# Optimization experiments

Hardware: AMD Instinct MI355X
Metric: run time of the kernel (lower is better)

The kernel has to match this reference:

```python
import jax, jax.numpy as jnp
import numpy as np

B, N, D_MODEL, D_INNER = 8, 1024, 512, 2048
N_HEAD, D_K, D_V = 8, 64, 64
N_EXPERTS, TOP_K = 24, 2
N_GROUPS = 4
EPS = 1e-6


def setup_inputs() -> dict:
    key = jax.random.key(0)
    ks = jax.random.split(key, 12)
    s = 0.02
    rn = lambda k, shp: jax.random.normal(k, shp, dtype=jnp.float32) * s
    inp = {
        "x": jax.random.normal(ks[0], (B, N, D_MODEL), dtype=jnp.float32),
        "wq": rn(ks[1], (D_MODEL, N_HEAD * D_K)),
        "wk": rn(ks[2], (D_MODEL, N_HEAD * D_K)),
        "wv": rn(ks[3], (D_MODEL, N_HEAD * D_V)),
        "wo": rn(ks[4], (N_HEAD * D_V, D_MODEL)),
        "ln_attn_g": jnp.ones((D_MODEL,), jnp.float32),
        "ln_attn_b": jnp.zeros((D_MODEL,), jnp.float32),
        "wg1": rn(ks[5], (D_MODEL, N_EXPERTS)),
        "w1": rn(ks[6], (N_EXPERTS, D_MODEL, D_INNER)),
        "b1": jnp.zeros((N_EXPERTS, D_INNER), jnp.float32),
        "wg2": rn(ks[7], (D_INNER, N_EXPERTS)),
        "w2": rn(ks[8], (N_EXPERTS, D_INNER, D_MODEL)),
        "b2": jnp.zeros((N_EXPERTS, D_MODEL), jnp.float32),
        "ln_out_g": jnp.ones((D_MODEL,), jnp.float32),
        "ln_out_b": jnp.zeros((D_MODEL,), jnp.float32),
    }
    for i in range(1, 5):
        inp[f"ln{i}_g"] = jnp.ones((D_INNER,), jnp.float32)
        inp[f"ln{i}_b"] = jnp.zeros((D_INNER,), jnp.float32)
    return inp


def _ln(x, g, b):
    m = jnp.mean(x, -1, keepdims=True)
    v = jnp.mean((x - m) ** 2, -1, keepdims=True)
    return (x - m) * jax.lax.rsqrt(v + EPS) * g + b


def _gate(xf, wg, capacity):
    # top-2 gating with capacity-limited one-hot dispatch (GShard-style)
    gates = jax.nn.softmax(xf @ wg)                      # [T,E]
    w, idx = jax.lax.top_k(gates, TOP_K)                 # [T,2]
    w = w / jnp.sum(w, -1, keepdims=True)
    m1 = jax.nn.one_hot(idx[:, 0], N_EXPERTS, dtype=xf.dtype)
    m2 = jax.nn.one_hot(idx[:, 1], N_EXPERTS, dtype=xf.dtype)
    loc1 = jnp.cumsum(m1, 0) - 1.0                       # slot within expert
    loc2 = jnp.cumsum(m2, 0) - 1.0 + jnp.sum(m1, 0)[None, :]
    m1 = m1 * (loc1 < capacity)
    m2 = m2 * (loc2 < capacity)
    c1 = w[:, 0, None, None] * m1[:, :, None] * jax.nn.one_hot(loc1.astype(jnp.int32), capacity, dtype=xf.dtype)
    c2 = w[:, 1, None, None] * m2[:, :, None] * jax.nn.one_hot(loc2.astype(jnp.int32), capacity, dtype=xf.dtype)
    combine = c1 + c2                                    # [T,E,C]
    dispatch = (combine > 0).astype(xf.dtype)
    return combine, dispatch


def _moe(xf, combine, dispatch, W, b):
    ein = jnp.einsum('tec,td->ecd', dispatch, xf)        # gather into expert slots
    out = jnp.einsum('ecd,edh->ech', ein, W) + b[:, None, :]
    return jnp.einsum('tec,ech->th', combine, out)       # weighted combine


def reference(x, wq, wk, wv, wo, ln_attn_g, ln_attn_b, wg1, w1, b1, wg2, w2, b2,
              ln1_g, ln1_b, ln2_g, ln2_b, ln3_g, ln3_b, ln4_g, ln4_b,
              ln_out_g, ln_out_b):
    # ---- multi-head self-attention ----
    temp = D_K ** 0.5
    q = (x @ wq).reshape(B, N, N_HEAD, D_K)
    k = (x @ wk).reshape(B, N, N_HEAD, D_K)
    v = (x @ wv).reshape(B, N, N_HEAD, D_V)
    attn = jax.nn.softmax(jnp.einsum('bnhd,bmhd->bhnm', q / temp, k), axis=-1)
    ctx = jnp.einsum('bhnm,bmhd->bnhd', attn, v).reshape(B, N, N_HEAD * D_V)
    ctx = jax.nn.relu(ctx @ wo) + x                      # dropout is identity at eval
    ctx = _ln(ctx, ln_attn_g, ln_attn_b)
    # ---- TaskMoE positionwise FFN over 4 sequence groups ----
    resid = ctx
    xg = ctx.reshape(B, N_GROUPS, N // N_GROUPS, D_MODEL)
    T = B * (N // N_GROUPS)
    cap = int(np.ceil(T * TOP_K / N_EXPERTS))
    ln_gs = [ln1_g, ln2_g, ln3_g, ln4_g]
    ln_bs = [ln1_b, ln2_b, ln3_b, ln4_b]
    outs = []
    for i in range(N_GROUPS):
        xf = xg[:, i].reshape(T, D_MODEL)
        combine, dispatch = _gate(xf, wg1, cap)          # routing reused by 2nd MoE
        h = _moe(xf, combine, dispatch, w1, b1)          # [T, D_INNER]
        h = jax.nn.relu(_ln(h, ln_gs[i], ln_bs[i]))
        o = _moe(h, combine, dispatch, w2, b2)           # [T, D_MODEL]
        outs.append(o.reshape(B, N // N_GROUPS, D_MODEL))
    y = jnp.concatenate(outs, axis=1) + resid
    return _ln(y, ln_out_g, ln_out_b)
```

## Files before the change

kernel.cpp:

```cpp
#include <hip/hip_runtime.h>
#include <cstdint>


#define NTOK 8192
#define DM   512
#define DI   2048
#define NEXP 24
#define TPG  2048
#define CAP  171
#define CAPR 176
#define EPSF 1e-6f

typedef __bf16 bf16x8 __attribute__((ext_vector_type(8)));
typedef float f32x4 __attribute__((ext_vector_type(4)));

static __device__ __forceinline__ unsigned short f2bf(float f) {
  unsigned int u = __builtin_bit_cast(unsigned int, f);
  u = (u + 0x7fffu + ((u >> 16) & 1u)) >> 16;
  return (unsigned short)u;
}
static __device__ __forceinline__ unsigned int pk2(float a, float b) {
  return (unsigned int)f2bf(a) | ((unsigned int)f2bf(b) << 16);
}

static __device__ __forceinline__ void gload16(const unsigned short* g, unsigned short* l) {
  __builtin_amdgcn_global_load_lds(
      (const __attribute__((address_space(1))) void*)g,
      (__attribute__((address_space(3))) void*)l, 16, 0, 0);
}

__global__ __launch_bounds__(256) void convw(
    const float* __restrict__ in, unsigned short* __restrict__ out, int K, int N)
{
  __shared__ unsigned short T[64][65];
  int e = blockIdx.z;
  const float* ip = in + (size_t)e * K * N;
  unsigned short* op = out + (size_t)e * N * K;
  int n0 = blockIdx.x * 64, k0 = blockIdx.y * 64;
  int tid = threadIdx.x;
  #pragma unroll
  for (int i = 0; i < 16; ++i) {
    int lin = tid + i * 256;
    int k = lin >> 6, n = lin & 63;
    T[n][k] = f2bf(ip[(size_t)(k0 + k) * N + n0 + n]);
  }
  __syncthreads();
  #pragma unroll
  for (int i = 0; i < 16; ++i) {
    int lin = tid + i * 256;
    int n = lin >> 6, k = lin & 63;
    op[(size_t)(n0 + n) * K + k0 + k] = T[n][k];
  }
}

__global__ __launch_bounds__(256) void convx(
    const float* __restrict__ in, unsigned short* __restrict__ out)
{
  int i = blockIdx.x * 256 + threadIdx.x;
  float4 v = ((const float4*)in)[i];
  uint2 p;
  p.x = pk2(v.x, v.y); p.y = pk2(v.z, v.w);
  ((uint2*)out)[i] = p;
}

__global__ __launch_bounds__(256) void mfma_gemm(
    const unsigned short* __restrict__ A, int lda,
    const unsigned short* __restrict__ Bt,
    const float* __restrict__ bias,
    const int* __restrict__ lrow, const float* __restrict__ lw,
    const int* __restrict__ cnts,
    float* __restrict__ Cf, unsigned short* __restrict__ Cb,
    const float* __restrict__ Add,
    int M, int N, int K, int mode, float scale)
{
  __shared__ unsigned short As[2][64 * 64];
  __shared__ unsigned short Bs[2][128 * 64];
  int tid = threadIdx.x;
  int w = tid >> 6, lane = tid & 63, quad = lane >> 4, l16 = lane & 15;
  int n0 = blockIdx.x * 128;
  int m0 = blockIdx.y * 64;
  int pair = blockIdx.z;
  int e = pair % NEXP;
  int count = cnts ? cnts[pair] : M;
  if (m0 >= count) return;
  const int*   lr  = lrow ? lrow + pair * CAPR : nullptr;
  const float* lwp = lw   ? lw   + pair * CAPR : nullptr;

  int sub = lane >> 3;
  int gsw = (lane & 7) ^ sub;
  const unsigned short* aSrc[2];
  #pragma unroll
  for (int i = 0; i < 2; ++i) {
    int mm = m0 + i * 32 + w * 8 + sub;
    if (mm >= count) mm = count - 1;
    int rm = lr ? lr[mm] : mm;
    aSrc[i] = A + (size_t)rm * lda + gsw * 8;
  }
  const unsigned short* Bte = Bt + (size_t)e * N * K;
  const unsigned short* bSrc[4];
  #pragma unroll
  for (int i = 0; i < 4; ++i)
    bSrc[i] = Bte + (size_t)(n0 + i * 32 + w * 8 + sub) * K + gsw * 8;

  int wbase = w * 512;

  f32x4 acc[4][2] = {};
  int nt = K >> 6;

  #pragma unroll
  for (int i = 0; i < 2; ++i) gload16(aSrc[i], &As[0][i * 2048 + wbase]);
  #pragma unroll
  for (int i = 0; i < 4; ++i) gload16(bSrc[i], &Bs[0][i * 2048 + wbase]);

  for (int t = 0; t < nt; ++t) {
    asm volatile("s_waitcnt vmcnt(0)" ::: "memory");
    __syncthreads();
    int cur = t & 1;
    if (t + 1 < nt) {
      int koff = (t + 1) << 6;
      int nxt = cur ^ 1;
      #pragma unroll
      for (int i = 0; i < 2; ++i) gload16(aSrc[i] + koff, &As[nxt][i * 2048 + wbase]);
      #pragma unroll
      for (int i = 0; i < 4; ++i) gload16(bSrc[i] + koff, &Bs[nxt][i * 2048 + wbase]);
    }
    const unsigned short* Ab = As[cur];
    const unsigned short* Bb = Bs[cur];
    #pragma unroll
    for (int half = 0; half < 2; ++half) {
      int g8 = ((half * 4 + quad) ^ (l16 & 7)) * 8;
      bf16x8 af[4];
      #pragma unroll
      for (int ms = 0; ms < 4; ++ms)
        af[ms] = *(const bf16x8*)&Ab[(ms * 16 + l16) * 64 + g8];
      bf16x8 bfr[2];
      #pragma unroll
      for (int ns = 0; ns < 2; ++ns)
        bfr[ns] = *(const bf16x8*)&Bb[(w * 32 + ns * 16 + l16) * 64 + g8];
      #pragma unroll
      for (int ms = 0; ms < 4; ++ms)
        #pragma unroll
        for (int ns = 0; ns < 2; ++ns)
          acc[ms][ns] = __builtin_amdgcn_mfma_f32_16x16x32_bf16(af[ms], bfr[ns], acc[ms][ns], 0, 0, 0);
    }
  }
  float bv[2];
  if (mode == 2) {
    #pragma unroll
    for (int ns = 0; ns < 2; ++ns)
      bv[ns] = bias[(size_t)e * N + n0 + w * 32 + ns * 16 + l16];
  }
  #pragma unroll
  for (int ms = 0; ms < 4; ++ms) {
    #pragma unroll
    for (int ns = 0; ns < 2; ++ns) {
      int col = n0 + w * 32 + ns * 16 + l16;
      #pragma unroll
      for (int r = 0; r < 4; ++r) {
        int m = m0 + ms * 16 + quad * 4 + r;
        if (mode == 0) {
          Cb[(size_t)m * N + col] = f2bf(acc[ms][ns][r] * scale);
        } else if (mode == 1) {
          Cf[(size_t)m * N + col] = fmaxf(acc[ms][ns][r], 0.f) + Add[(size_t)m * N + col];
        } else {
          if (m < count) {
            int rr = lr[m];
            float wgt = lwp[m];
            atomicAdd(&Cf[(size_t)rr * N + col], wgt * (acc[ms][ns][r] + bv[ns]));
          }
        }
      }
    }
  }
}

__global__ __launch_bounds__(256) void attn_mfma(
    const unsigned short* __restrict__ Qb, const unsigned short* __restrict__ Kb,
    const unsigned short* __restrict__ Vb, unsigned short* __restrict__ ctx)
{
  __shared__ unsigned short Ks[64 * 72];
  __shared__ unsigned short Vt[64 * 72];
  __shared__ unsigned short Ps[4][16 * 72];
  int tid = threadIdx.x;
  int w = tid >> 6, lane = tid & 63, quad = lane >> 4, l16 = lane & 15;
  int qt = blockIdx.x, bh = blockIdx.y;
  int b = bh >> 3, h = bh & 7;
  size_t hoff = (size_t)h * 64;
  size_t tokbase = (size_t)b * 1024;

  int qrow = qt * 64 + w * 16 + l16;
  const unsigned short* qp = Qb + (tokbase + qrow) * 512 + hoff + quad * 8;
  bf16x8 qa0 = *(const bf16x8*)(qp);
  bf16x8 qa1 = *(const bf16x8*)(qp + 32);

  f32x4 O[4] = {};
  float mrow[4], lrowv[4];
  #pragma unroll
  for (int r = 0; r < 4; ++r) { mrow[r] = -1e30f; lrowv[r] = 0.f; }

  for (int kv0 = 0; kv0 < 1024; kv0 += 64) {
    __syncthreads();
    {
      const unsigned short* kg = Kb + (tokbase + kv0) * 512 + hoff;
      #pragma unroll
      for (int i = 0; i < 2; ++i) {
        int f = tid + i * 256;
        int key = f >> 3, c = f & 7;
        *(uint4*)&Ks[key * 72 + c * 8] = *(const uint4*)(kg + (size_t)key * 512 + c * 8);
      }
      const unsigned short* vg = Vb + (tokbase + kv0) * 512 + hoff;
      int d = tid & 63;
      #pragma unroll
      for (int i = 0; i < 2; ++i) {
        int ko = (tid >> 6) + i * 4;
        const unsigned short* vq = vg + (size_t)ko * 8 * 512 + d;
        unsigned int a0 = vq[0],        a1 = vq[512];
        unsigned int a2 = vq[2 * 512],  a3 = vq[3 * 512];
        unsigned int a4 = vq[4 * 512],  a5 = vq[5 * 512];
        unsigned int a6 = vq[6 * 512],  a7 = vq[7 * 512];
        uint4 pk;
        pk.x = a0 | (a1 << 16); pk.y = a2 | (a3 << 16);
        pk.z = a4 | (a5 << 16); pk.w = a6 | (a7 << 16);
        *(uint4*)&Vt[d * 72 + ko * 8] = pk;
      }
    }
    __syncthreads();

    f32x4 s[4];
    #pragma unroll
    for (int kt = 0; kt < 4; ++kt) {
      const unsigned short* kr = &Ks[(kt * 16 + l16) * 72 + quad * 8];
      bf16x8 kb0 = *(const bf16x8*)(kr);
      bf16x8 kb1 = *(const bf16x8*)(kr + 32);
      f32x4 z = {};
      z = __builtin_amdgcn_mfma_f32_16x16x32_bf16(qa0, kb0, z, 0, 0, 0);
      z = __builtin_amdgcn_mfma_f32_16x16x32_bf16(qa1, kb1, z, 0, 0, 0);
      s[kt] = z;
    }

    #pragma unroll
    for (int r = 0; r < 4; ++r) {
      float mx = fmaxf(fmaxf(s[0][r], s[1][r]), fmaxf(s[2][r], s[3][r]));
      mx = fmaxf(mx, __shfl_xor(mx, 1, 64));
      mx = fmaxf(mx, __shfl_xor(mx, 2, 64));
      mx = fmaxf(mx, __shfl_xor(mx, 4, 64));
      mx = fmaxf(mx, __shfl_xor(mx, 8, 64));
      float mnew = fmaxf(mrow[r], mx);
      float alpha = __expf(mrow[r] - mnew);
      mrow[r] = mnew;
      float psum = 0.f;
      #pragma unroll
      for (int kt = 0; kt < 4; ++kt) {
        float p = __expf(s[kt][r] - mnew);
        s[kt][r] = p;
        psum += p;
      }
      psum += __shfl_xor(psum, 1, 64);
      psum += __shfl_xor(psum, 2, 64);
      psum += __shfl_xor(psum, 4, 64);
      psum += __shfl_xor(psum, 8, 64);
      lrowv[r] = lrowv[r] * alpha + psum;
      #pragma unroll
      for (int dt = 0; dt < 4; ++dt) O[dt][r] *= alpha;
    }

    #pragma unroll
    for (int kt = 0; kt < 4; ++kt)
      #pragma unroll
      for (int r = 0; r < 4; ++r)
        Ps[w][(quad * 4 + r) * 72 + kt * 16 + l16] = f2bf(s[kt][r]);
    const unsigned short* pp = &Ps[w][l16 * 72 + quad * 8];
    bf16x8 pa0 = *(const bf16x8*)(pp);
    bf16x8 pa1 = *(const bf16x8*)(pp + 32);

    #pragma unroll
    for (int dt = 0; dt < 4; ++dt) {
      const unsigned short* vr = &Vt[(dt * 16 + l16) * 72 + quad * 8];
      bf16x8 vb0 = *(const bf16x8*)(vr);
      bf16x8 vb1 = *(const bf16x8*)(vr + 32);
      O[dt] = __builtin_amdgcn_mfma_f32_16x16x32_bf16(pa0, vb0, O[dt], 0, 0, 0);
      O[dt] = __builtin_amdgcn_mfma_f32_16x16x32_bf16(pa1, vb1, O[dt], 0, 0, 0);
    }
  }

  #pragma unroll
  for (int r = 0; r < 4; ++r) {
    float inv = 1.0f / lrowv[r];
    int row = qt * 64 + w * 16 + quad * 4 + r;
    unsigned short* cp = ctx + (tokbase + row) * 512 + hoff + l16;
    #pragma unroll
    for (int dt = 0; dt < 4; ++dt) cp[dt * 16] = f2bf(O[dt][r] * inv);
  }
}

__global__ __launch_bounds__(256) void ln_kernel(
    const float* __restrict__ in, const float* __restrict__ add,
    float* __restrict__ out, unsigned short* __restrict__ outb,
    int D, int relu_after,
    const float* __restrict__ g0, const float* __restrict__ g1,
    const float* __restrict__ g2, const float* __restrict__ g3,
    const float* __restrict__ bb0, const float* __restrict__ bb1,
    const float* __restrict__ bb2, const float* __restrict__ bb3)
{
  int row = blockIdx.x;
  int grp = (row & 1023) >> 8;
  const float* g  = grp == 0 ? g0  : grp == 1 ? g1  : grp == 2 ? g2  : g3;
  const float* bb = grp == 0 ? bb0 : grp == 1 ? bb1 : grp == 2 ? bb2 : bb3;
  const float* ip = in + (size_t)row * D;
  const float* ap = add ? add + (size_t)row * D : nullptr;
  float vals[8];
  int per = D >> 8;
  float s1 = 0.f, s2 = 0.f;
  for (int i = 0; i < per; ++i) {
    int d = threadIdx.x + (i << 8);
    float vv = ip[d];
    if (ap) vv += ap[d];
    vals[i] = vv; s1 += vv; s2 += vv * vv;
  }
  #pragma unroll
  for (int o = 32; o; o >>= 1) { s1 += __shfl_xor(s1, o, 64); s2 += __shfl_xor(s2, o, 64); }
  __shared__ float sA[4], sB[4];
  int wid = threadIdx.x >> 6, lane = threadIdx.x & 63;
  if (lane == 0) { sA[wid] = s1; sB[wid] = s2; }
  __syncthreads();
  float t1 = sA[0] + sA[1] + sA[2] + sA[3];
  float t2 = sB[0] + sB[1] + sB[2] + sB[3];
  float mean = t1 / (float)D;
  float var = t2 / (float)D - mean * mean;
  float rs = rsqrtf(var + EPSF);
  float* op = out ? out + (size_t)row * D : nullptr;
  unsigned short* obp = outb ? outb + (size_t)row * D : nullptr;
  for (int i = 0; i < per; ++i) {
    int d = threadIdx.x + (i << 8);
    float o = (vals[i] - mean) * rs * g[d] + bb[d];
    if (relu_after) o = fmaxf(o, 0.f);
    if (op)  op[d] = o;
    if (obp) obp[d] = f2bf(o);
  }
}

__global__ __launch_bounds__(256) void gate1(
    const float* __restrict__ xln, const float* __restrict__ wg,
    int* __restrict__ idx0, int* __restrict__ idx1,
    float* __restrict__ w0o, float* __restrict__ w1o)
{
  int wid = threadIdx.x >> 6, lane = threadIdx.x & 63;
  int tk = blockIdx.x * 4 + wid;
  int g = tk >> 11, t = tk & 2047;
  int b = t >> 8, j = t & 255;
  size_t row = (size_t)b * 1024 + g * 256 + j;
  const float* xp = xln + row * 512;
  float acc = -1e30f;
  if (lane < 24) {
    acc = 0.f;
    for (int d = 0; d < 512; ++d) acc += xp[d] * wg[d * 24 + lane];
  }
  float b0v = -1e30f, b1v = -1e30f; int i0 = 0, i1 = 0;
  for (int e = 0; e < 24; ++e) {
    float vv = __shfl(acc, e, 64);
    if (vv > b0v)      { b1v = b0v; i1 = i0; b0v = vv; i0 = e; }
    else if (vv > b1v) { b1v = vv; i1 = e; }
  }
  if (lane == 0) {
    float w0 = 1.0f / (1.0f + __expf(b1v - b0v));
    idx0[tk] = i0; idx1[tk] = i1; w0o[tk] = w0; w1o[tk] = 1.0f - w0;
  }
}

__global__ __launch_bounds__(64) void gate2(
    const int* __restrict__ idx0, const int* __restrict__ idx1,
    const float* __restrict__ w0, const float* __restrict__ w1,
    int* __restrict__ lrow, float* __restrict__ lw, int* __restrict__ counts)
{
  int pair = blockIdx.x; int g = pair / 24; int e = pair % 24;
  int lane = threadIdx.x;
  int base = g * TPG;
  unsigned long long lm = (lane == 63) ? 0x7fffffffffffffffULL : ((1ULL << lane) - 1ULL);
  int run = 0;
  for (int it = 0; it < TPG / 64; ++it) {
    int t = it * 64 + lane;
    bool m = (idx0[base + t] == e);
    unsigned long long mask = __ballot(m);
    int pre = __popcll(mask & lm);
    int rank = run + pre;
    if (m && rank < CAP) {
      int bq = t >> 8, j = t & 255;
      lrow[pair * CAPR + rank] = bq * 1024 + g * 256 + j;
      lw[pair * CAPR + rank] = w0[base + t];
    }
    run += __popcll(mask);
  }
  int total1 = run;
  int run2 = 0;
  for (int it = 0; it < TPG / 64; ++it) {
    int t = it * 64 + lane;
    bool m = (idx1[base + t] == e);
    unsigned long long mask = __ballot(m);
    int pre = __popcll(mask & lm);
    int rank2 = run2 + pre;
    if (m && (total1 + rank2) < CAP) {
      int bq = t >> 8, j = t & 255;
      lrow[pair * CAPR + total1 + rank2] = bq * 1024 + g * 256 + j;
      lw[pair * CAPR + total1 + rank2] = w1[base + t];
    }
    run2 += __popcll(mask);
  }
  if (lane == 0) {
    int c1 = total1 < CAP ? total1 : CAP;
    int room = CAP - total1; if (room < 0) room = 0;
    int c2 = run2 < room ? run2 : room;
    counts[pair] = c1 + c2;
  }
}

extern "C" void kernel_launch(void* const* d_in, const int* in_sizes, int n_in,
                              void* d_out, int out_size, void* d_ws, size_t ws_size,
                              hipStream_t stream)
{
  const float* x   = (const float*)d_in[0];
  const float* wq  = (const float*)d_in[1];
  const float* wk  = (const float*)d_in[2];
  const float* wv  = (const float*)d_in[3];
  const float* wo  = (const float*)d_in[4];
  const float* ln_attn_g = (const float*)d_in[5];
  const float* ln_attn_b = (const float*)d_in[6];
  const float* wg1 = (const float*)d_in[7];
  const float* w1  = (const float*)d_in[8];
  const float* b1  = (const float*)d_in[9];
  const float* w2  = (const float*)d_in[11];
  const float* b2  = (const float*)d_in[12];
  const float* ln_out_g = (const float*)d_in[13];
  const float* ln_out_b = (const float*)d_in[14];
  const float* ln1g = (const float*)d_in[15]; const float* ln1b = (const float*)d_in[16];
  const float* ln2g = (const float*)d_in[17]; const float* ln2b = (const float*)d_in[18];
  const float* ln3g = (const float*)d_in[19]; const float* ln3b = (const float*)d_in[20];
  const float* ln4g = (const float*)d_in[21]; const float* ln4b = (const float*)d_in[22];

  char* ws = (char*)d_ws;
  const size_t MB = 1048576;
  unsigned short* wt1  = (unsigned short*)(ws + 0);
  unsigned short* wtq  = (unsigned short*)(ws + 48 * MB);
  unsigned short* wtk  = (unsigned short*)(ws + 48 * MB + 524288);
  unsigned short* wtv  = (unsigned short*)(ws + 49 * MB);
  unsigned short* wto  = (unsigned short*)(ws + 49 * MB + 524288);
  unsigned short* xbf  = (unsigned short*)(ws + 50 * MB);
  unsigned short* hb2  = (unsigned short*)(ws + 50 * MB);
  unsigned short* qbf  = (unsigned short*)(ws + 58 * MB);
  unsigned short* kbf  = (unsigned short*)(ws + 66 * MB);
  unsigned short* vbf  = (unsigned short*)(ws + 74 * MB);
  unsigned short* ctxb = (unsigned short*)(ws + 82 * MB);
  float* y0    = (float*)(ws + 90 * MB);
  float* ymoe  = (float*)(ws + 90 * MB);
  float* ctxln = (float*)(ws + 106 * MB);
  unsigned short* ctxlnb = (unsigned short*)(ws + 122 * MB);
  float* hb    = (float*)(ws + 130 * MB);
  unsigned short* wt2 = (unsigned short*)(ws + 130 * MB);
  char*  small = ws + 194 * MB;
  int*   idx0  = (int*)(small + 0);
  int*   idx1  = (int*)(small + 32768);
  float* w0a   = (float*)(small + 65536);
  float* w1a   = (float*)(small + 98304);
  int*   lrowp = (int*)(small + 131072);
  float* lwv   = (float*)(small + 198656);
  int*   cnts  = (int*)(small + 266240);

  dim3 blk(256);
  convw<<<dim3(8, 8, 1), blk, 0, stream>>>(wq, wtq, 512, 512);
  convw<<<dim3(8, 8, 1), blk, 0, stream>>>(wk, wtk, 512, 512);
  convw<<<dim3(8, 8, 1), blk, 0, stream>>>(wv, wtv, 512, 512);
  convw<<<dim3(8, 8, 1), blk, 0, stream>>>(wo, wto, 512, 512);
  convw<<<dim3(32, 8, 24), blk, 0, stream>>>(w1, wt1, 512, 2048);
  convx<<<4096, blk, 0, stream>>>(x, xbf);
  mfma_gemm<<<dim3(4, 128, 1), blk, 0, stream>>>(xbf, DM, wtq, nullptr, nullptr, nullptr, nullptr,
      nullptr, qbf, nullptr, NTOK, DM, DM, 0, 0.125f);
  mfma_gemm<<<dim3(4, 128, 1), blk, 0, stream>>>(xbf, DM, wtk, nullptr, nullptr, nullptr, nullptr,
      nullptr, kbf, nullptr, NTOK, DM, DM, 0, 1.0f);
  mfma_gemm<<<dim3(4, 128, 1), blk, 0, stream>>>(xbf, DM, wtv, nullptr, nullptr, nullptr, nullptr,
      nullptr, vbf, nullptr, NTOK, DM, DM, 0, 1.0f);
  attn_mfma<<<dim3(16, 64), blk, 0, stream>>>(qbf, kbf, vbf, ctxb);
  mfma_gemm<<<dim3(4, 128, 1), blk, 0, stream>>>(ctxb, DM, wto, nullptr, nullptr, nullptr, nullptr,
      y0, nullptr, x, NTOK, DM, DM, 1, 1.0f);
  ln_kernel<<<8192, blk, 0, stream>>>(y0, nullptr, ctxln, ctxlnb, DM, 0,
      ln_attn_g, ln_attn_g, ln_attn_g, ln_attn_g, ln_attn_b, ln_attn_b, ln_attn_b, ln_attn_b);
  gate1<<<2048, blk, 0, stream>>>(ctxln, wg1, idx0, idx1, w0a, w1a);
  gate2<<<96, 64, 0, stream>>>(idx0, idx1, w0a, w1a, lrowp, lwv, cnts);
  hipMemsetAsync(hb, 0, (size_t)NTOK * DI * 4, stream);
  hipMemsetAsync(ymoe, 0, (size_t)NTOK * DM * 4, stream);
  mfma_gemm<<<dim3(16, 3, 96), blk, 0, stream>>>(ctxlnb, DM, wt1, b1, lrowp, lwv, cnts,
      hb, nullptr, nullptr, 0, DI, DM, 2, 1.0f);
  ln_kernel<<<8192, blk, 0, stream>>>(hb, nullptr, nullptr, hb2, DI, 1,
      ln1g, ln2g, ln3g, ln4g, ln1b, ln2b, ln3b, ln4b);
  convw<<<dim3(8, 32, 24), blk, 0, stream>>>(w2, wt2, 2048, 512);
  mfma_gemm<<<dim3(4, 3, 96), blk, 0, stream>>>(hb2, DI, wt2, b2, lrowp, lwv, cnts,
      ymoe, nullptr, nullptr, 0, DM, DI, 2, 1.0f);
  ln_kernel<<<8192, blk, 0, stream>>>(ymoe, ctxln, (float*)d_out, nullptr, DM, 0,
      ln_out_g, ln_out_g, ln_out_g, ln_out_g, ln_out_b, ln_out_b, ln_out_b, ln_out_b);
}
```

Baseline: 829.8 us.

## Replace atomic MoE scatter with slot buffers and gather-combine fused into layernorm

The expert GEMMs now write bf16 per-slot outputs instead of atomically adding weighted results into zeroed fp32 token buffers. New combine_ln kernels gather each token's two slots through token-to-slot maps built in gate2, apply the gate weights and residual, and run the layernorm in the same pass. This removes the large memsets and the atomic traffic. The Q/K/V projections are also merged into one GEMM with a packed 1536-wide output that attention reads directly. The GEMM drops its double-buffered LDS prefetch for a simpler load-wait-compute loop, which may expose memory latency, and the intermediate expert outputs are rounded to bf16 before combining.

```diff
diff --git a/kernel.cpp b/kernel.cpp
--- a/kernel.cpp
+++ b/kernel.cpp
@@ -19,6 +19,9 @@
   u = (u + 0x7fffu + ((u >> 16) & 1u)) >> 16;
   return (unsigned short)u;
 }
+static __device__ __forceinline__ float bf2f(unsigned short u) {
+  return __builtin_bit_cast(float, (unsigned int)u << 16);
+}
 static __device__ __forceinline__ unsigned int pk2(float a, float b) {
   return (unsigned int)f2bf(a) | ((unsigned int)f2bf(b) << 16);
 }
@@ -67,14 +70,13 @@
     const unsigned short* __restrict__ A, int lda,
     const unsigned short* __restrict__ Bt,
     const float* __restrict__ bias,
-    const int* __restrict__ lrow, const float* __restrict__ lw,
-    const int* __restrict__ cnts,
+    const int* __restrict__ lrow, const int* __restrict__ cnts,
     float* __restrict__ Cf, unsigned short* __restrict__ Cb,
     const float* __restrict__ Add,
     int M, int N, int K, int mode, float scale)
 {
-  __shared__ unsigned short As[2][64 * 64];
-  __shared__ unsigned short Bs[2][128 * 64];
+  __shared__ unsigned short As[64 * 64];
+  __shared__ unsigned short Bs[128 * 64];
   int tid = threadIdx.x;
   int w = tid >> 6, lane = tid & 63, quad = lane >> 4, l16 = lane & 15;
   int n0 = blockIdx.x * 128;
@@ -83,8 +85,7 @@
   int e = pair % NEXP;
   int count = cnts ? cnts[pair] : M;
   if (m0 >= count) return;
-  const int*   lr  = lrow ? lrow + pair * CAPR : nullptr;
-  const float* lwp = lw   ? lw   + pair * CAPR : nullptr;
+  const int* lr = lrow ? lrow + pair * CAPR : nullptr;
 
   int sub = lane >> 3;
   int gsw = (lane & 7) ^ sub;
@@ -105,38 +106,25 @@
   int wbase = w * 512;
 
   f32x4 acc[4][2] = {};
-  int nt = K >> 6;
-
-  #pragma unroll
-  for (int i = 0; i < 2; ++i) gload16(aSrc[i], &As[0][i * 2048 + wbase]);
-  #pragma unroll
-  for (int i = 0; i < 4; ++i) gload16(bSrc[i], &Bs[0][i * 2048 + wbase]);
-
-  for (int t = 0; t < nt; ++t) {
+  for (int t = 0; t < K; t += 64) {
+    if (t) __syncthreads();
+    #pragma unroll
+    for (int i = 0; i < 2; ++i) gload16(aSrc[i] + t, &As[i * 2048 + wbase]);
+    #pragma unroll
+    for (int i = 0; i < 4; ++i) gload16(bSrc[i] + t, &Bs[i * 2048 + wbase]);
     asm volatile("s_waitcnt vmcnt(0)" ::: "memory");
     __syncthreads();
-    int cur = t & 1;
-    if (t + 1 < nt) {
-      int koff = (t + 1) << 6;
-      int nxt = cur ^ 1;
-      #pragma unroll
-      for (int i = 0; i < 2; ++i) gload16(aSrc[i] + koff, &As[nxt][i * 2048 + wbase]);
-      #pragma unroll
-      for (int i = 0; i < 4; ++i) gload16(bSrc[i] + koff, &Bs[nxt][i * 2048 + wbase]);
-    }
-    const unsigned short* Ab = As[cur];
-    const unsigned short* Bb = Bs[cur];
     #pragma unroll
     for (int half = 0; half < 2; ++half) {
       int g8 = ((half * 4 + quad) ^ (l16 & 7)) * 8;
       bf16x8 af[4];
       #pragma unroll
       for (int ms = 0; ms < 4; ++ms)
-        af[ms] = *(const bf16x8*)&Ab[(ms * 16 + l16) * 64 + g8];
+        af[ms] = *(const bf16x8*)&As[(ms * 16 + l16) * 64 + g8];
       bf16x8 bfr[2];
       #pragma unroll
       for (int ns = 0; ns < 2; ++ns)
-        bfr[ns] = *(const bf16x8*)&Bb[(w * 32 + ns * 16 + l16) * 64 + g8];
+        bfr[ns] = *(const bf16x8*)&Bs[(w * 32 + ns * 16 + l16) * 64 + g8];
       #pragma unroll
       for (int ms = 0; ms < 4; ++ms)
         #pragma unroll
@@ -144,11 +132,13 @@
           acc[ms][ns] = __builtin_amdgcn_mfma_f32_16x16x32_bf16(af[ms], bfr[ns], acc[ms][ns], 0, 0, 0);
     }
   }
-  float bv[2];
-  if (mode == 2) {
+  float bv[2] = {0.f, 0.f};
+  unsigned short* Cbp = Cb;
+  if (mode == 3) {
     #pragma unroll
     for (int ns = 0; ns < 2; ++ns)
       bv[ns] = bias[(size_t)e * N + n0 + w * 32 + ns * 16 + l16];
+    Cbp = Cb + (size_t)pair * CAPR * N;
   }
   #pragma unroll
   for (int ms = 0; ms < 4; ++ms) {
@@ -159,15 +149,13 @@
       for (int r = 0; r < 4; ++r) {
         int m = m0 + ms * 16 + quad * 4 + r;
         if (mode == 0) {
-          Cb[(size_t)m * N + col] = f2bf(acc[ms][ns][r] * scale);
+          float sc = col < 512 ? scale : 1.0f;
+          Cbp[(size_t)m * N + col] = f2bf(acc[ms][ns][r] * sc);
         } else if (mode == 1) {
           Cf[(size_t)m * N + col] = fmaxf(acc[ms][ns][r], 0.f) + Add[(size_t)m * N + col];
         } else {
-          if (m < count) {
-            int rr = lr[m];
-            float wgt = lwp[m];
-            atomicAdd(&Cf[(size_t)rr * N + col], wgt * (acc[ms][ns][r] + bv[ns]));
-          }
+          if (m < CAPR)
+            Cbp[(size_t)m * N + col] = f2bf(acc[ms][ns][r] + bv[ns]);
         }
       }
     }
@@ -175,8 +163,7 @@
 }
 
 __global__ __launch_bounds__(256) void attn_mfma(
-    const unsigned short* __restrict__ Qb, const unsigned short* __restrict__ Kb,
-    const unsigned short* __restrict__ Vb, unsigned short* __restrict__ ctx)
+    const unsigned short* __restrict__ QKV, unsigned short* __restrict__ ctx)
 {
   __shared__ unsigned short Ks[64 * 72];
   __shared__ unsigned short Vt[64 * 72];
@@ -189,7 +176,7 @@
   size_t tokbase = (size_t)b * 1024;
 
   int qrow = qt * 64 + w * 16 + l16;
-  const unsigned short* qp = Qb + (tokbase + qrow) * 512 + hoff + quad * 8;
+  const unsigned short* qp = QKV + (tokbase + qrow) * 1536 + hoff + quad * 8;
   bf16x8 qa0 = *(const bf16x8*)(qp);
   bf16x8 qa1 = *(const bf16x8*)(qp + 32);
 
@@ -201,23 +188,23 @@
   for (int kv0 = 0; kv0 < 1024; kv0 += 64) {
     __syncthreads();
     {
-      const unsigned short* kg = Kb + (tokbase + kv0) * 512 + hoff;
+      const unsigned short* kg = QKV + (tokbase + kv0) * 1536 + 512 + hoff;
       #pragma unroll
       for (int i = 0; i < 2; ++i) {
         int f = tid + i * 256;
         int key = f >> 3, c = f & 7;
-        *(uint4*)&Ks[key * 72 + c * 8] = *(const uint4*)(kg + (size_t)key * 512 + c * 8);
+        *(uint4*)&Ks[key * 72 + c * 8] = *(const uint4*)(kg + (size_t)key * 1536 + c * 8);
       }
-      const unsigned short* vg = Vb + (tokbase + kv0) * 512 + hoff;
+      const unsigned short* vg = QKV + (tokbase + kv0) * 1536 + 1024 + hoff;
       int d = tid & 63;
       #pragma unroll
       for (int i = 0; i < 2; ++i) {
         int ko = (tid >> 6) + i * 4;
-        const unsigned short* vq = vg + (size_t)ko * 8 * 512 + d;
-        unsigned int a0 = vq[0],        a1 = vq[512];
-        unsigned int a2 = vq[2 * 512],  a3 = vq[3 * 512];
-        unsigned int a4 = vq[4 * 512],  a5 = vq[5 * 512];
-        unsigned int a6 = vq[6 * 512],  a7 = vq[7 * 512];
+        const unsigned short* vq = vg + (size_t)ko * 8 * 1536 + d;
+        unsigned int a0 = vq[0],         a1 = vq[1536];
+        unsigned int a2 = vq[2 * 1536],  a3 = vq[3 * 1536];
+        unsigned int a4 = vq[4 * 1536],  a5 = vq[5 * 1536];
+        unsigned int a6 = vq[6 * 1536],  a7 = vq[7 * 1536];
         uint4 pk;
         pk.x = a0 | (a1 << 16); pk.y = a2 | (a3 << 16);
         pk.z = a4 | (a5 << 16); pk.w = a6 | (a7 << 16);
@@ -294,27 +281,18 @@
 }
 
 __global__ __launch_bounds__(256) void ln_kernel(
-    const float* __restrict__ in, const float* __restrict__ add,
+    const float* __restrict__ in,
     float* __restrict__ out, unsigned short* __restrict__ outb,
-    int D, int relu_after,
-    const float* __restrict__ g0, const float* __restrict__ g1,
-    const float* __restrict__ g2, const float* __restrict__ g3,
-    const float* __restrict__ bb0, const float* __restrict__ bb1,
-    const float* __restrict__ bb2, const float* __restrict__ bb3)
+    int D, const float* __restrict__ g, const float* __restrict__ bb)
 {
   int row = blockIdx.x;
-  int grp = (row & 1023) >> 8;
-  const float* g  = grp == 0 ? g0  : grp == 1 ? g1  : grp == 2 ? g2  : g3;
-  const float* bb = grp == 0 ? bb0 : grp == 1 ? bb1 : grp == 2 ? bb2 : bb3;
   const float* ip = in + (size_t)row * D;
-  const float* ap = add ? add + (size_t)row * D : nullptr;
   float vals[8];
   int per = D >> 8;
   float s1 = 0.f, s2 = 0.f;
   for (int i = 0; i < per; ++i) {
     int d = threadIdx.x + (i << 8);
     float vv = ip[d];
-    if (ap) vv += ap[d];
     vals[i] = vv; s1 += vv; s2 += vv * vv;
   }
   #pragma unroll
@@ -333,6 +311,63 @@
   for (int i = 0; i < per; ++i) {
     int d = threadIdx.x + (i << 8);
     float o = (vals[i] - mean) * rs * g[d] + bb[d];
+    if (op)  op[d] = o;
+    if (obp) obp[d] = f2bf(o);
+  }
+}
+
+template<int PER>
+__global__ __launch_bounds__(256) void combine_ln(
+    const unsigned short* __restrict__ slots,
+    const int* __restrict__ ts0, const int* __restrict__ ts1,
+    const float* __restrict__ sw,
+    const float* __restrict__ addf,
+    float* __restrict__ outf, unsigned short* __restrict__ outb,
+    int relu_after,
+    const float* __restrict__ g0, const float* __restrict__ g1,
+    const float* __restrict__ g2, const float* __restrict__ g3,
+    const float* __restrict__ bb0, const float* __restrict__ bb1,
+    const float* __restrict__ bb2, const float* __restrict__ bb3)
+{
+  const int D = PER * 256;
+  int row = blockIdx.x;
+  int grp = (row & 1023) >> 8;
+  const float* g  = grp == 0 ? g0  : grp == 1 ? g1  : grp == 2 ? g2  : g3;
+  const float* bb = grp == 0 ? bb0 : grp == 1 ? bb1 : grp == 2 ? bb2 : bb3;
+  int s0 = ts0[row], s1 = ts1[row];
+  float w0 = s0 >= 0 ? sw[s0] : 0.f;
+  float w1 = s1 >= 0 ? sw[s1] : 0.f;
+  const unsigned short* p0 = slots + (size_t)(s0 >= 0 ? s0 : 0) * D;
+  const unsigned short* p1 = slots + (size_t)(s1 >= 0 ? s1 : 0) * D;
+  const float* ap = addf ? addf + (size_t)row * D : nullptr;
+  int base = threadIdx.x * PER;
+  float vals[PER];
+  float sm1 = 0.f, sm2 = 0.f;
+  #pragma unroll
+  for (int i = 0; i < PER; ++i) {
+    int d = base + i;
+    float v = ap ? ap[d] : 0.f;
+    if (s0 >= 0) v += w0 * bf2f(p0[d]);
+    if (s1 >= 0) v += w1 * bf2f(p1[d]);
+    vals[i] = v; sm1 += v; sm2 += v * v;
+  }
+  #pragma unroll
+  for (int o = 32; o; o >>= 1) { sm1 += __shfl_xor(sm1, o, 64); sm2 += __shfl_xor(sm2, o, 64); }
+  __shared__ float sA[4], sB[4];
+  int wid = threadIdx.x >> 6, lane = threadIdx.x & 63;
+  if (lane == 0) { sA[wid] = sm1; sB[wid] = sm2; }
+  __syncthreads();
+  float t1 = sA[0] + sA[1] + sA[2] + sA[3];
+  float t2 = sB[0] + sB[1] + sB[2] + sB[3];
+  float mean = t1 / (float)D;
+  float var = t2 / (float)D - mean * mean;
+  float rs = rsqrtf(var + EPSF);
+  float* op = outf ? outf + (size_t)row * D : nullptr;
+  unsigned short* obp = outb ? outb + (size_t)row * D : nullptr;
+  #pragma unroll
+  for (int i = 0; i < PER; ++i) {
+    int d = base + i;
+    float o = (vals[i] - mean) * rs * g[d] + bb[d];
     if (relu_after) o = fmaxf(o, 0.f);
     if (op)  op[d] = o;
     if (obp) obp[d] = f2bf(o);
@@ -370,7 +405,8 @@
 __global__ __launch_bounds__(64) void gate2(
     const int* __restrict__ idx0, const int* __restrict__ idx1,
     const float* __restrict__ w0, const float* __restrict__ w1,
-    int* __restrict__ lrow, float* __restrict__ lw, int* __restrict__ counts)
+    int* __restrict__ lrow, float* __restrict__ lw, int* __restrict__ counts,
+    int* __restrict__ ts0, int* __restrict__ ts1)
 {
   int pair = blockIdx.x; int g = pair / 24; int e = pair % 24;
   int lane = threadIdx.x;
@@ -385,8 +421,10 @@
     int rank = run + pre;
     if (m && rank < CAP) {
       int bq = t >> 8, j = t & 255;
-      lrow[pair * CAPR + rank] = bq * 1024 + g * 256 + j;
+      int rowidx = bq * 1024 + g * 256 + j;
+      lrow[pair * CAPR + rank] = rowidx;
       lw[pair * CAPR + rank] = w0[base + t];
+      ts0[rowidx] = pair * CAPR + rank;
     }
     run += __popcll(mask);
   }
@@ -400,8 +438,10 @@
     int rank2 = run2 + pre;
     if (m && (total1 + rank2) < CAP) {
       int bq = t >> 8, j = t & 255;
-      lrow[pair * CAPR + total1 + rank2] = bq * 1024 + g * 256 + j;
+      int rowidx = bq * 1024 + g * 256 + j;
+      lrow[pair * CAPR + total1 + rank2] = rowidx;
       lw[pair * CAPR + total1 + rank2] = w1[base + t];
+      ts1[rowidx] = pair * CAPR + total1 + rank2;
     }
     run2 += __popcll(mask);
   }
@@ -438,24 +478,20 @@
 
   char* ws = (char*)d_ws;
   const size_t MB = 1048576;
-  unsigned short* wt1  = (unsigned short*)(ws + 0);
-  unsigned short* wtq  = (unsigned short*)(ws + 48 * MB);
-  unsigned short* wtk  = (unsigned short*)(ws + 48 * MB + 524288);
-  unsigned short* wtv  = (unsigned short*)(ws + 49 * MB);
-  unsigned short* wto  = (unsigned short*)(ws + 49 * MB + 524288);
-  unsigned short* xbf  = (unsigned short*)(ws + 50 * MB);
-  unsigned short* hb2  = (unsigned short*)(ws + 50 * MB);
-  unsigned short* qbf  = (unsigned short*)(ws + 58 * MB);
-  unsigned short* kbf  = (unsigned short*)(ws + 66 * MB);
-  unsigned short* vbf  = (unsigned short*)(ws + 74 * MB);
-  unsigned short* ctxb = (unsigned short*)(ws + 82 * MB);
-  float* y0    = (float*)(ws + 90 * MB);
-  float* ymoe  = (float*)(ws + 90 * MB);
-  float* ctxln = (float*)(ws + 106 * MB);
-  unsigned short* ctxlnb = (unsigned short*)(ws + 122 * MB);
-  float* hb    = (float*)(ws + 130 * MB);
-  unsigned short* wt2 = (unsigned short*)(ws + 130 * MB);
-  char*  small = ws + 194 * MB;
+  unsigned short* wt1    = (unsigned short*)(ws + 0);
+  unsigned short* hb2    = (unsigned short*)(ws + 0);
+  unsigned short* wt2    = (unsigned short*)(ws + 48 * MB);
+  float*          ctxln  = (float*)(ws + 96 * MB);
+  unsigned short* ctxlnb = (unsigned short*)(ws + 112 * MB);
+  unsigned short* xbf    = (unsigned short*)(ws + 120 * MB);
+  unsigned short* out1   = (unsigned short*)(ws + 120 * MB);
+  unsigned short* out2   = (unsigned short*)(ws + 120 * MB);
+  unsigned short* qkvb   = (unsigned short*)(ws + 128 * MB);
+  unsigned short* ctxb   = (unsigned short*)(ws + 152 * MB);
+  unsigned short* wtqkv  = (unsigned short*)(ws + 160 * MB);
+  unsigned short* wto    = (unsigned short*)(ws + 160 * MB + 1572864);
+  float*          y0     = (float*)(ws + 162 * MB);
+  char*  small = ws + 190 * MB;
   int*   idx0  = (int*)(small + 0);
   int*   idx1  = (int*)(small + 32768);
   float* w0a   = (float*)(small + 65536);
@@ -463,36 +499,33 @@
   int*   lrowp = (int*)(small + 131072);
   float* lwv   = (float*)(small + 198656);
   int*   cnts  = (int*)(small + 266240);
+  int*   ts0   = (int*)(small + 270336);
+  int*   ts1   = (int*)(small + 303104);
 
   dim3 blk(256);
-  convw<<<dim3(8, 8, 1), blk, 0, stream>>>(wq, wtq, 512, 512);
-  convw<<<dim3(8, 8, 1), blk, 0, stream>>>(wk, wtk, 512, 512);
-  convw<<<dim3(8, 8, 1), blk, 0, stream>>>(wv, wtv, 512, 512);
+  convw<<<dim3(8, 8, 1), blk, 0, stream>>>(wq, wtqkv, 512, 512);
+  convw<<<dim3(8, 8, 1), blk, 0, stream>>>(wk, wtqkv + (size_t)512 * 512, 512, 512);
+  convw<<<dim3(8, 8, 1), blk, 0, stream>>>(wv, wtqkv + (size_t)1024 * 512, 512, 512);
   convw<<<dim3(8, 8, 1), blk, 0, stream>>>(wo, wto, 512, 512);
   convw<<<dim3(32, 8, 24), blk, 0, stream>>>(w1, wt1, 512, 2048);
+  convw<<<dim3(8, 32, 24), blk, 0, stream>>>(w2, wt2, 2048, 512);
   convx<<<4096, blk, 0, stream>>>(x, xbf);
-  mfma_gemm<<<dim3(4, 128, 1), blk, 0, stream>>>(xbf, DM, wtq, nullptr, nullptr, nullptr, nullptr,
-      nullptr, qbf, nullptr, NTOK, DM, DM, 0, 0.125f);
-  mfma_gemm<<<dim3(4, 128, 1), blk, 0, stream>>>(xbf, DM, wtk, nullptr, nullptr, nullptr, nullptr,
-      nullptr, kbf, nullptr, NTOK, DM, DM, 0, 1.0f);
-  mfma_gemm<<<dim3(4, 128, 1), blk, 0, stream>>>(xbf, DM, wtv, nullptr, nullptr, nullptr, nullptr,
-      nullptr, vbf, nullptr, NTOK, DM, DM, 0, 1.0f);
-  attn_mfma<<<dim3(16, 64), blk, 0, stream>>>(qbf, kbf, vbf, ctxb);
-  mfma_gemm<<<dim3(4, 128, 1), blk, 0, stream>>>(ctxb, DM, wto, nullptr, nullptr, nullptr, nullptr,
+  mfma_gemm<<<dim3(12, 128, 1), blk, 0, stream>>>(xbf, DM, wtqkv, nullptr, nullptr, nullptr,
+      nullptr, qkvb, nullptr, NTOK, 1536, DM, 0, 0.125f);
+  attn_mfma<<<dim3(16, 64), blk, 0, stream>>>(qkvb, ctxb);
+  mfma_gemm<<<dim3(4, 128, 1), blk, 0, stream>>>(ctxb, DM, wto, nullptr, nullptr, nullptr,
       y0, nullptr, x, NTOK, DM, DM, 1, 1.0f);
-  ln_kernel<<<8192, blk, 0, stream>>>(y0, nullptr, ctxln, ctxlnb, DM, 0,
-      ln_attn_g, ln_attn_g, ln_attn_g, ln_attn_g, ln_attn_b, ln_attn_b, ln_attn_b, ln_attn_b);
+  ln_kernel<<<8192, blk, 0, stream>>>(y0, ctxln, ctxlnb, DM, ln_attn_g, ln_attn_b);
   gate1<<<2048, blk, 0, stream>>>(ctxln, wg1, idx0, idx1, w0a, w1a);
-  gate2<<<96, 64, 0, stream>>>(idx0, idx1, w0a, w1a, lrowp, lwv, cnts);
-  hipMemsetAsync(hb, 0, (size_t)NTOK * DI * 4, stream);
-  hipMemsetAsync(ymoe, 0, (size_t)NTOK * DM * 4, stream);
-  mfma_gemm<<<dim3(16, 3, 96), blk, 0, stream>>>(ctxlnb, DM, wt1, b1, lrowp, lwv, cnts,
-      hb, nullptr, nullptr, 0, DI, DM, 2, 1.0f);
-  ln_kernel<<<8192, blk, 0, stream>>>(hb, nullptr, nullptr, hb2, DI, 1,
-      ln1g, ln2g, ln3g, ln4g, ln1b, ln2b, ln3b, ln4b);
-  convw<<<dim3(8, 32, 24), blk, 0, stream>>>(w2, wt2, 2048, 512);
-  mfma_gemm<<<dim3(4, 3, 96), blk, 0, stream>>>(hb2, DI, wt2, b2, lrowp, lwv, cnts,
-      ymoe, nullptr, nullptr, 0, DM, DI, 2, 1.0f);
-  ln_kernel<<<8192, blk, 0, stream>>>(ymoe, ctxln, (float*)d_out, nullptr, DM, 0,
-      ln_out_g, ln_out_g, ln_out_g, ln_out_g, ln_out_b, ln_out_b, ln_out_b, ln_out_b);
-}
+  hipMemsetAsync(ts0, 0xFF, 65536, stream);
+  gate2<<<96, 64, 0, stream>>>(idx0, idx1, w0a, w1a, lrowp, lwv, cnts, ts0, ts1);
+  mfma_gemm<<<dim3(16, 3, 96), blk, 0, stream>>>(ctxlnb, DM, wt1, b1, lrowp, cnts,
+      nullptr, out1, nullptr, 0, DI, DM, 3, 1.0f);
+  combine_ln<8><<<8192, blk, 0, stream>>>(out1, ts0, ts1, lwv, nullptr,
+      nullptr, hb2, 1, ln1g, ln2g, ln3g, ln4g, ln1b, ln2b, ln3b, ln4b);
+  mfma_gemm<<<dim3(4, 3, 96), blk, 0, stream>>>(hb2, DI, wt2, b2, lrowp, cnts,
+      nullptr, out2, nullptr, 0, DM, DI, 3, 1.0f);
+  combine_ln<2><<<8192, blk, 0, stream>>>(out2, ts0, ts1, lwv, ctxln,
+      (float*)d_out, nullptr, 0, ln_out_g, ln_out_g, ln_out_g, ln_out_g,
+      ln_out_b, ln_out_b, ln_out_b, ln_out_b);
+}
```

After: 776.4 us. 1.07x faster.
